# Kernel optimization log

Measured on AMD Instinct MI355X. Metric: run time of the kernel, lower is better.

The kernel has to match this reference:

```python
import jax, jax.numpy as jnp
import numpy as np

N = 50000      # nodes
E = 800000     # edges
G = 50         # graphs in batch
F_IN = 64      # num_node_features
HID = 128      # hidden_dim
EMB = 64       # embed_dim
H1 = 8         # heads layer 1
C1 = HID // H1 # per-head channels layer 1
NCLS = 6
EPS = 1e-5
NEG_SLOPE = 0.2


def setup_inputs() -> dict:
    key = jax.random.key(0)
    ks = jax.random.split(key, 26)
    rn = lambda k, s, sc=0.1: jax.random.normal(k, s, jnp.float32) * sc
    return {
        "x": jax.random.normal(ks[0], (N, F_IN), jnp.float32),
        "edge_index": jax.random.randint(ks[1], (2, E), 0, N),
        "edge_attr": jax.random.uniform(ks[2], (E, 1), dtype=jnp.float32),
        "batch": jnp.sort(jax.random.randint(ks[3], (N,), 0, G)),
        # conv1 (GATv2, heads=8, concat)
        "Wl1": rn(ks[4], (F_IN, HID)), "bl1": jnp.zeros((HID,), jnp.float32),
        "Wr1": rn(ks[5], (F_IN, HID)), "br1": jnp.zeros((HID,), jnp.float32),
        "We1": rn(ks[6], (1, HID)),
        "att1": rn(ks[7], (H1, C1)), "bias1": jnp.zeros((HID,), jnp.float32),
        # conv2 (GATv2, heads=1, mean)
        "Wl2": rn(ks[8], (HID, EMB)), "bl2": jnp.zeros((EMB,), jnp.float32),
        "Wr2": rn(ks[9], (HID, EMB)), "br2": jnp.zeros((EMB,), jnp.float32),
        "We2": rn(ks[10], (1, EMB)),
        "att2": rn(ks[11], (1, EMB)), "bias2": jnp.zeros((EMB,), jnp.float32),
        # batchnorms
        "gamma1": jnp.ones((HID,), jnp.float32), "beta1": jnp.zeros((HID,), jnp.float32),
        "gamma2": jnp.ones((EMB,), jnp.float32), "beta2": jnp.zeros((EMB,), jnp.float32),
        # classifier
        "Wc": rn(ks[12], (EMB, NCLS)), "bc": jnp.zeros((NCLS,), jnp.float32),
    }


def _segment_softmax(logits, seg, n):
    # logits: [E, H], softmax over edges sharing the same destination node
    m = jax.ops.segment_max(logits, seg, num_segments=n)
    e = jnp.exp(logits - m[seg])
    s = jax.ops.segment_sum(e, seg, num_segments=n)
    return e / s[seg]


def _gatv2(x, src, dst, eattr, Wl, bl, Wr, br, We, att, bias, H, C, concat):
    n = x.shape[0]
    xl = (x @ Wl + bl).reshape(n, H, C)   # source transform (messages)
    xr = (x @ Wr + br).reshape(n, H, C)   # target transform
    ee = (eattr @ We).reshape(-1, H, C)   # edge feature embedding
    g = jax.nn.leaky_relu(xl[src] + xr[dst] + ee, NEG_SLOPE)  # [E,H,C]
    alpha = jnp.einsum('ehc,hc->eh', g, att)                  # [E,H]
    alpha = _segment_softmax(alpha, dst, n)
    out = jax.ops.segment_sum(xl[src] * alpha[:, :, None], dst, num_segments=n)
    out = out.reshape(n, H * C) if concat else out.mean(axis=1)
    return out + bias


def _add_self_loops(edge_index, eattr, n):
    # PyG add_self_loops with fill_value='mean': self-loop edge_attr = mean of
    # incoming edge_attr per node (0 if isolated)
    src, dst = edge_index[0], edge_index[1]
    deg = jax.ops.segment_sum(jnp.ones((src.shape[0],), jnp.float32), dst, num_segments=n)
    s = jax.ops.segment_sum(eattr, dst, num_segments=n)
    loop_attr = jnp.where(deg[:, None] > 0, s / jnp.maximum(deg, 1.0)[:, None], 0.0)
    ar = jnp.arange(n)
    return (jnp.concatenate([src, ar]), jnp.concatenate([dst, ar]),
            jnp.concatenate([eattr, loop_attr], axis=0))


def _bn_train(x, gamma, beta):
    mu = x.mean(axis=0)
    var = x.var(axis=0)  # biased, as BatchNorm uses for normalization
    return (x - mu) * jax.lax.rsqrt(var + EPS) * gamma + beta


def reference(x, edge_index, edge_attr, batch,
              Wl1, bl1, Wr1, br1, We1, att1, bias1,
              Wl2, bl2, Wr2, br2, We2, att2, bias2,
              gamma1, beta1, gamma2, beta2, Wc, bc):
    src, dst, ea = _add_self_loops(edge_index, edge_attr, N)
    h = _gatv2(x, src, dst, ea, Wl1, bl1, Wr1, br1, We1, att1, bias1, H1, C1, True)
    h = jax.nn.relu(_bn_train(h, gamma1, beta1))
    h = _gatv2(h, src, dst, ea, Wl2, bl2, Wr2, br2, We2, att2, bias2, 1, EMB, False)
    node_emb = jax.nn.relu(_bn_train(h, gamma2, beta2))
    cnt = jax.ops.segment_sum(jnp.ones((N,), jnp.float32), batch, num_segments=G)
    domain_emb = jax.ops.segment_sum(node_emb, batch, num_segments=G) / jnp.maximum(cnt, 1.0)[:, None]
    logits = domain_emb @ Wc + bc
    return (logits, domain_emb, node_emb)
```

## Files before the change

kernel.cpp:

```cpp
#include <hip/hip_runtime.h>
#include <hip/hip_bf16.h>
#include <math.h>

#define NN 50000
#define EE 800000
#define GG 50
#define FIN 64
#define HID 128
#define EMB 64
#define NCLS 6
#define EPSBN 1e-5f
#define NEG 0.2f
#define MAXD 64

__device__ __forceinline__ float lrelu(float x){ return x > 0.f ? x : NEG * x; }
__device__ __forceinline__ float bf16lo(unsigned u){ return __uint_as_float(u << 16); }
__device__ __forceinline__ float bf16hi(unsigned u){ return __uint_as_float(u & 0xffff0000u); }
__device__ __forceinline__ unsigned f2bf_bits(float f){
    unsigned u = __float_as_uint(f);
    return (u + 0x7fffu + ((u >> 16) & 1u)) >> 16;
}

__global__ void k_scatter(const int* __restrict__ ei, const float* __restrict__ ea,
                          unsigned long long* __restrict__ combo,
                          unsigned* __restrict__ epack) {
    int e = blockIdx.x * 256 + threadIdx.x;
    if (e < EE) {
        int d = ei[EE + e];
        int s = ei[e];
        float eaf = ea[e];
        unsigned long long add = (1ULL << 40) | (unsigned long long)(eaf * 1048576.0f);
        unsigned long long old = atomicAdd(&combo[d], add);
        int pos = (int)(old >> 40);
        epack[d * MAXD + pos] = ((unsigned)s << 16) | f2bf_bits(eaf);
    }
}

__global__ void k_decode(const unsigned long long* __restrict__ combo,
                         int* __restrict__ deg, float* __restrict__ loopattr) {
    int n = blockIdx.x * 256 + threadIdx.x;
    if (n < NN) {
        unsigned long long c = combo[n];
        int cnt = (int)(c >> 40);
        float easum = (float)(c & ((1ULL << 40) - 1)) * (1.0f / 1048576.0f);
        deg[n] = cnt;
        loopattr[n] = cnt > 0 ? easum / (float)cnt : 0.f;
    }
}

__global__ void k_bounds(const int* __restrict__ batch, int* __restrict__ gstart) {
    int n = blockIdx.x * 256 + threadIdx.x;
    if (n < NN) {
        int b = batch[n];
        int prev = (n == 0) ? -1 : batch[n - 1];
        for (int g = prev + 1; g <= b; g++) gstart[g] = n;
        if (n == NN - 1) {
            for (int g = b + 1; g <= GG; g++) gstart[g] = NN;
        }
    }
}

#define G1R 8
__global__ void k_gemm1(const float* __restrict__ x,
                        const float* __restrict__ Wl, const float* __restrict__ bl,
                        const float* __restrict__ Wr, const float* __restrict__ br,
                        __hip_bfloat16* __restrict__ xlh, float* __restrict__ xr) {
    __shared__ float xs[G1R][FIN];
    int rb = blockIdx.x * G1R;
    int t = threadIdx.x;
    for (int i = t; i < G1R * FIN; i += 256) {
        int r = i >> 6, k = i & 63;
        xs[r][k] = x[(rb + r) * FIN + k];
    }
    __syncthreads();
    bool isL = t < HID;
    int c = isL ? t : t - HID;
    const float* W = isL ? Wl : Wr;
    float bias = isL ? bl[c] : br[c];
    float acc[G1R];
#pragma unroll
    for (int r = 0; r < G1R; r++) acc[r] = bias;
    for (int k = 0; k < FIN; k++) {
        float w = W[k * HID + c];
#pragma unroll
        for (int r = 0; r < G1R; r++) acc[r] += xs[r][k] * w;
    }
    if (isL) {
#pragma unroll
        for (int r = 0; r < G1R; r++) xlh[(rb + r) * HID + c] = __float2bfloat16(acc[r]);
    } else {
#pragma unroll
        for (int r = 0; r < G1R; r++) xr[(rb + r) * HID + c] = acc[r];
    }
}

__global__ void k_gat1(const float* __restrict__ loopattr, const int* __restrict__ deg,
                       const unsigned* __restrict__ epack,
                       const __hip_bfloat16* __restrict__ xlh, const float* __restrict__ xr1,
                       const float* __restrict__ We1, const float* __restrict__ att1,
                       const float* __restrict__ bias1, float* __restrict__ out1) {
    int wid = (blockIdx.x * blockDim.x + threadIdx.x) >> 6;
    int lane = threadIdx.x & 63;
    if (wid >= NN) return;
    int n = wid;
    int half = lane >> 5;
    int cl   = lane & 31;
    int c0   = 4 * cl;
    float4 xrv = *reinterpret_cast<const float4*>(&xr1[n * HID + c0]);
    float4 we  = *reinterpret_cast<const float4*>(&We1[c0]);
    float4 at  = *reinterpret_cast<const float4*>(&att1[c0]);
    float la = loopattr[n];
    int beg = n * MAXD, end = beg + deg[n];

    float m0 = -INFINITY, s0 = 0.f, a00 = 0.f, a01 = 0.f, a02 = 0.f, a03 = 0.f;
    float m1 = -INFINITY, s1 = 0.f, a10 = 0.f, a11 = 0.f, a12 = 0.f, a13 = 0.f;

#define UPD1(U, EA, MM, SS, A0, A1, A2, A3)                                   \
    {                                                                          \
        float x0 = bf16lo((U).x), x1 = bf16hi((U).x);                          \
        float x2 = bf16lo((U).y), x3 = bf16hi((U).y);                          \
        float g0 = lrelu(x0 + xrv.x + (EA) * we.x);                            \
        float g1 = lrelu(x1 + xrv.y + (EA) * we.y);                            \
        float g2 = lrelu(x2 + xrv.z + (EA) * we.z);                            \
        float g3 = lrelu(x3 + xrv.w + (EA) * we.w);                            \
        float part = g0 * at.x + g1 * at.y + g2 * at.z + g3 * at.w;            \
        part += __shfl_xor(part, 1);                                           \
        part += __shfl_xor(part, 2);                                           \
        float mnew = fmaxf(MM, part);                                          \
        float sc = __expf(MM - mnew);                                          \
        float p  = __expf(part - mnew);                                        \
        SS = SS * sc + p;                                                      \
        A0 = A0 * sc + x0 * p;                                                 \
        A1 = A1 * sc + x1 * p;                                                 \
        A2 = A2 * sc + x2 * p;                                                 \
        A3 = A3 * sc + x3 * p;                                                 \
        MM = mnew;                                                             \
    }

    for (int base = beg; base < end; base += 4) {
        int i0 = base + half;
        int i1 = i0 + 2;
        bool act0 = i0 < end;
        bool act1 = i1 < end;
        unsigned q0 = act0 ? epack[i0] : 0u;
        unsigned q1 = act1 ? epack[i1] : 0u;
        uint2 u0 = act0 ? *reinterpret_cast<const uint2*>(&xlh[(q0 >> 16) * HID + c0]) : make_uint2(0, 0);
        uint2 u1 = act1 ? *reinterpret_cast<const uint2*>(&xlh[(q1 >> 16) * HID + c0]) : make_uint2(0, 0);
        if (act0) UPD1(u0, bf16lo(q0), m0, s0, a00, a01, a02, a03);
        if (act1) UPD1(u1, bf16lo(q1), m1, s1, a10, a11, a12, a13);
    }
    if (half == 1) {
        uint2 u = *reinterpret_cast<const uint2*>(&xlh[n * HID + c0]);
        UPD1(u, la, m0, s0, a00, a01, a02, a03);
    }
#undef UPD1

    {
        float mm = fmaxf(m0, m1);
        float e0 = (m0 > -INFINITY) ? __expf(m0 - mm) : 0.f;
        float e1 = (m1 > -INFINITY) ? __expf(m1 - mm) : 0.f;
        s0 = s0 * e0 + s1 * e1;
        a00 = a00 * e0 + a10 * e1;
        a01 = a01 * e0 + a11 * e1;
        a02 = a02 * e0 + a12 * e1;
        a03 = a03 * e0 + a13 * e1;
        m0 = mm;
    }
    {
        float mo = __shfl_xor(m0, 32);
        float so = __shfl_xor(s0, 32);
        float b0 = __shfl_xor(a00, 32);
        float b1 = __shfl_xor(a01, 32);
        float b2 = __shfl_xor(a02, 32);
        float b3 = __shfl_xor(a03, 32);
        float mm = fmaxf(m0, mo);
        float e0 = (m0 > -INFINITY) ? __expf(m0 - mm) : 0.f;
        float e1 = (mo > -INFINITY) ? __expf(mo - mm) : 0.f;
        s0 = s0 * e0 + so * e1;
        a00 = a00 * e0 + b0 * e1;
        a01 = a01 * e0 + b1 * e1;
        a02 = a02 * e0 + b2 * e1;
        a03 = a03 * e0 + b3 * e1;
    }
    if (half == 0) {
        float4 bi = *reinterpret_cast<const float4*>(&bias1[c0]);
        float inv = 1.f / s0;
        float4 o = make_float4(a00 * inv + bi.x, a01 * inv + bi.y,
                               a02 * inv + bi.z, a03 * inv + bi.w);
        *reinterpret_cast<float4*>(&out1[n * HID + c0]) = o;
    }
}

template <int CH>
__global__ void k_bnstat(const float* __restrict__ xin, float* __restrict__ sums,
                         float* __restrict__ sumsq) {
    constexpr int RPI = 256 / CH;
    int t = threadIdx.x;
    int c = t % CH;
    int rl = t / CH;
    float s = 0.f, q = 0.f;
    for (int r = blockIdx.x * RPI + rl; r < NN; r += gridDim.x * RPI) {
        float v = xin[r * CH + c];
        s += v; q += v * v;
    }
    __shared__ float sh[256], shq[256];
    sh[t] = s; shq[t] = q;
    __syncthreads();
    if (t < CH) {
        float ts = 0.f, tq = 0.f;
        for (int i = t; i < 256; i += CH) { ts += sh[i]; tq += shq[i]; }
        atomicAdd(&sums[c], ts);
        atomicAdd(&sumsq[c], tq);
    }
}

template <int CH>
__global__ void k_bnfin(const float* __restrict__ sums, const float* __restrict__ sumsq,
                        const float* __restrict__ gamma, const float* __restrict__ beta,
                        float* __restrict__ a, float* __restrict__ b) {
    int c = threadIdx.x;
    if (c < CH) {
        float mean = sums[c] / (float)NN;
        float var  = sumsq[c] / (float)NN - mean * mean;
        float rs = rsqrtf(var + EPSBN);
        float aa = gamma[c] * rs;
        a[c] = aa;
        b[c] = beta[c] - mean * aa;
    }
}

#define G2R 8
__global__ void k_gemm2(const float* __restrict__ out1, const float* __restrict__ a1,
                        const float* __restrict__ b1,
                        const float* __restrict__ Wl, const float* __restrict__ bl,
                        const float* __restrict__ Wr, const float* __restrict__ br,
                        __hip_bfloat16* __restrict__ xlh, float* __restrict__ xr2) {
    __shared__ float hs[G2R][HID];
    int rb = blockIdx.x * G2R;
    int t = threadIdx.x;
    for (int i = t; i < G2R * HID; i += 256) {
        int r = i >> 7, k = i & 127;
        float v = out1[(rb + r) * HID + k] * a1[k] + b1[k];
        hs[r][k] = v > 0.f ? v : 0.f;
    }
    __syncthreads();
    int c = t & 127;
    int rg = (t >> 7) * 4;
    bool isL = c < EMB;
    int cc = isL ? c : c - EMB;
    const float* W = isL ? Wl : Wr;
    float bias = isL ? bl[cc] : br[cc];
    float acc[4] = {bias, bias, bias, bias};
    for (int k = 0; k < HID; k++) {
        float w = W[k * EMB + cc];
#pragma unroll
        for (int r = 0; r < 4; r++) acc[r] += hs[rg + r][k] * w;
    }
    if (isL) {
#pragma unroll
        for (int r = 0; r < 4; r++) xlh[(rb + rg + r) * EMB + cc] = __float2bfloat16(acc[r]);
    } else {
#pragma unroll
        for (int r = 0; r < 4; r++) xr2[(rb + rg + r) * EMB + cc] = acc[r];
    }
}

__global__ void k_gat2(const float* __restrict__ loopattr, const int* __restrict__ deg,
                       const unsigned* __restrict__ epack,
                       const __hip_bfloat16* __restrict__ xlh, const float* __restrict__ xr2,
                       const float* __restrict__ We2, const float* __restrict__ att2,
                       const float* __restrict__ bias2, float* __restrict__ out2) {
    int wid = (blockIdx.x * blockDim.x + threadIdx.x) >> 6;
    int lane = threadIdx.x & 63;
    if (wid >= NN) return;
    int n = wid;
    int half = lane >> 5;
    int cl   = lane & 31;
    int c0   = 2 * cl;
    float2 xrv = *reinterpret_cast<const float2*>(&xr2[n * EMB + c0]);
    float2 we  = *reinterpret_cast<const float2*>(&We2[c0]);
    float2 at  = *reinterpret_cast<const float2*>(&att2[c0]);
    float la = loopattr[n];
    int beg = n * MAXD, end = beg + deg[n];

    float m0 = -INFINITY, s0 = 0.f, a00 = 0.f, a01 = 0.f;
    float m1 = -INFINITY, s1 = 0.f, a10 = 0.f, a11 = 0.f;

#define UPD2(U, EA, MM, SS, A0, A1)                                           \
    {                                                                          \
        float x0 = bf16lo(U), x1 = bf16hi(U);                                  \
        float g0 = lrelu(x0 + xrv.x + (EA) * we.x);                            \
        float g1 = lrelu(x1 + xrv.y + (EA) * we.y);                            \
        float part = g0 * at.x + g1 * at.y;                                    \
        part += __shfl_xor(part, 1);                                           \
        part += __shfl_xor(part, 2);                                           \
        part += __shfl_xor(part, 4);                                           \
        part += __shfl_xor(part, 8);                                           \
        part += __shfl_xor(part, 16);                                          \
        float mnew = fmaxf(MM, part);                                          \
        float sc = __expf(MM - mnew);                                          \
        float p  = __expf(part - mnew);                                        \
        SS = SS * sc + p;                                                      \
        A0 = A0 * sc + x0 * p;                                                 \
        A1 = A1 * sc + x1 * p;                                                 \
        MM = mnew;                                                             \
    }

    for (int base = beg; base < end; base += 4) {
        int i0 = base + half;
        int i1 = i0 + 2;
        bool act0 = i0 < end;
        bool act1 = i1 < end;
        unsigned q0 = act0 ? epack[i0] : 0u;
        unsigned q1 = act1 ? epack[i1] : 0u;
        unsigned u0 = act0 ? *reinterpret_cast<const unsigned*>(&xlh[(q0 >> 16) * EMB + c0]) : 0u;
        unsigned u1 = act1 ? *reinterpret_cast<const unsigned*>(&xlh[(q1 >> 16) * EMB + c0]) : 0u;
        if (act0) UPD2(u0, bf16lo(q0), m0, s0, a00, a01);
        if (act1) UPD2(u1, bf16lo(q1), m1, s1, a10, a11);
    }
    if (half == 1) {
        unsigned u = *reinterpret_cast<const unsigned*>(&xlh[n * EMB + c0]);
        UPD2(u, la, m0, s0, a00, a01);
    }
#undef UPD2

    {
        float mm = fmaxf(m0, m1);
        float e0 = (m0 > -INFINITY) ? __expf(m0 - mm) : 0.f;
        float e1 = (m1 > -INFINITY) ? __expf(m1 - mm) : 0.f;
        s0 = s0 * e0 + s1 * e1;
        a00 = a00 * e0 + a10 * e1;
        a01 = a01 * e0 + a11 * e1;
        m0 = mm;
    }
    {
        float mo = __shfl_xor(m0, 32);
        float so = __shfl_xor(s0, 32);
        float b0 = __shfl_xor(a00, 32);
        float b1 = __shfl_xor(a01, 32);
        float mm = fmaxf(m0, mo);
        float e0 = (m0 > -INFINITY) ? __expf(m0 - mm) : 0.f;
        float e1 = (mo > -INFINITY) ? __expf(mo - mm) : 0.f;
        s0 = s0 * e0 + so * e1;
        a00 = a00 * e0 + b0 * e1;
        a01 = a01 * e0 + b1 * e1;
    }
    if (half == 0) {
        float inv = 1.f / s0;
        float2 o = make_float2(a00 * inv + bias2[c0], a01 * inv + bias2[c0 + 1]);
        *reinterpret_cast<float2*>(&out2[n * EMB + c0]) = o;
    }
}

__global__ void k_emb(const float* __restrict__ out2, const float* __restrict__ a2,
                      const float* __restrict__ b2, float* __restrict__ nodeemb) {
    int i = blockIdx.x * 256 + threadIdx.x;
    if (i < NN * EMB) {
        int c = i & 63;
        float v = out2[i] * a2[c] + b2[c];
        nodeemb[i] = v > 0.f ? v : 0.f;
    }
}

__global__ void k_pool(const float* __restrict__ nodeemb, const int* __restrict__ gstart,
                       const float* __restrict__ Wc, const float* __restrict__ bc,
                       float* __restrict__ dom, float* __restrict__ logits) {
    int g = blockIdx.x;
    int t = threadIdx.x;
    int c = t & 63, rl = t >> 6;
    int beg = gstart[g], end = gstart[g + 1];
    float s = 0.f;
    for (int r = beg + rl; r < end; r += 4) s += nodeemb[r * EMB + c];
    __shared__ float sh[256];
    __shared__ float dsh[EMB];
    sh[t] = s;
    __syncthreads();
    if (t < EMB) {
        float tot = sh[t] + sh[t + 64] + sh[t + 128] + sh[t + 192];
        float cf = (float)(end - beg);
        if (cf < 1.f) cf = 1.f;
        float d = tot / cf;
        dsh[t] = d;
        dom[g * EMB + t] = d;
    }
    __syncthreads();
    if (t < NCLS) {
        float acc = bc[t];
        for (int k = 0; k < EMB; k++) acc += dsh[k] * Wc[k * NCLS + t];
        logits[g * NCLS + t] = acc;
    }
}

extern "C" void kernel_launch(void* const* d_in, const int* in_sizes, int n_in,
                              void* d_out, int out_size, void* d_ws, size_t ws_size,
                              hipStream_t stream) {
    const float* x     = (const float*)d_in[0];
    const int*   ei    = (const int*)d_in[1];
    const float* ea    = (const float*)d_in[2];
    const int*   batch = (const int*)d_in[3];
    const float* Wl1 = (const float*)d_in[4];
    const float* bl1 = (const float*)d_in[5];
    const float* Wr1 = (const float*)d_in[6];
    const float* br1 = (const float*)d_in[7];
    const float* We1 = (const float*)d_in[8];
    const float* att1 = (const float*)d_in[9];
    const float* bias1 = (const float*)d_in[10];
    const float* Wl2 = (const float*)d_in[11];
    const float* bl2 = (const float*)d_in[12];
    const float* Wr2 = (const float*)d_in[13];
    const float* br2 = (const float*)d_in[14];
    const float* We2 = (const float*)d_in[15];
    const float* att2 = (const float*)d_in[16];
    const float* bias2 = (const float*)d_in[17];
    const float* gamma1 = (const float*)d_in[18];
    const float* beta1  = (const float*)d_in[19];
    const float* gamma2 = (const float*)d_in[20];
    const float* beta2  = (const float*)d_in[21];
    const float* Wc = (const float*)d_in[22];
    const float* bc = (const float*)d_in[23];

    float* out_logits = (float*)d_out;
    float* out_dom    = out_logits + GG * NCLS;
    float* out_emb    = out_dom + GG * EMB;

    char* ws = (char*)d_ws;
    const size_t SZF = (size_t)NN * HID * sizeof(float);
    const size_t SZH = (size_t)NN * HID * sizeof(__hip_bfloat16);
    const size_t SZE = (size_t)NN * MAXD * sizeof(unsigned);
    __hip_bfloat16* xl1h = (__hip_bfloat16*)(ws);
    float* xr1  = (float*)(ws + SZH);
    float* out1 = (float*)(ws + SZH + SZF);
    __hip_bfloat16* xl2h = xl1h;
    float* xr2  = xr1;
    float* out2 = out1;
    unsigned* epack = (unsigned*)(ws + SZH + 2 * SZF);
    int*   deg      = (int*)(ws + SZH + 2 * SZF + SZE);
    float* loopattr = (float*)(deg + NN);
    unsigned long long* combo = (unsigned long long*)(loopattr + NN);
    float* sums1  = (float*)(combo + NN);
    float* sumsq1 = sums1 + HID;
    float* sums2  = sumsq1 + HID;
    float* sumsq2 = sums2 + EMB;
    size_t zero_bytes = (char*)(sumsq2 + EMB) - (char*)combo;
    float* a1 = (float*)(sumsq2 + EMB);
    float* b1 = a1 + HID;
    float* a2 = b1 + HID;
    float* b2 = a2 + EMB;
    int* gstart = (int*)(b2 + EMB);

    hipMemsetAsync(combo, 0, zero_bytes, stream);

    k_scatter<<<(EE + 255) / 256, 256, 0, stream>>>(ei, ea, combo, epack);
    k_decode<<<(NN + 255) / 256, 256, 0, stream>>>(combo, deg, loopattr);
    k_bounds<<<(NN + 255) / 256, 256, 0, stream>>>(batch, gstart);

    k_gemm1<<<NN / G1R, 256, 0, stream>>>(x, Wl1, bl1, Wr1, br1, xl1h, xr1);
    k_gat1<<<(NN * 64) / 256, 256, 0, stream>>>(loopattr, deg, epack,
                                                xl1h, xr1, We1, att1, bias1, out1);
    k_bnstat<HID><<<1024, 256, 0, stream>>>(out1, sums1, sumsq1);
    k_bnfin<HID><<<1, HID, 0, stream>>>(sums1, sumsq1, gamma1, beta1, a1, b1);
    k_gemm2<<<NN / G2R, 256, 0, stream>>>(out1, a1, b1, Wl2, bl2, Wr2, br2, xl2h, xr2);
    k_gat2<<<(NN * 64) / 256, 256, 0, stream>>>(loopattr, deg, epack,
                                                xl2h, xr2, We2, att2, bias2, out2);
    k_bnstat<EMB><<<1024, 256, 0, stream>>>(out2, sums2, sumsq2);
    k_bnfin<EMB><<<1, EMB, 0, stream>>>(sums2, sumsq2, gamma2, beta2, a2, b2);
    k_emb<<<(NN * EMB + 255) / 256, 256, 0, stream>>>(out2, a2, b2, out_emb);
    k_pool<<<GG, 256, 0, stream>>>(out_emb, gstart, Wc, bc, out_dom, out_logits);
}
```

Before: 499.3 us.

## Drop online-softmax max tracking, fuse decode/bounds, and fuse emb with pooling

Removes the running-max rescaling in both GAT aggregation kernels and accumulates exp(logit) directly, which makes the half-wave and cross-half merges plain sums. Merges the degree decode and graph-bounds kernels into one launch. Folds the BN2 apply and ReLU into a parallel pooling kernel (several blocks per graph, atomics into a zeroed buffer) followed by a small logits kernel, so the node-embedding pass is no longer split across two launches. Skipping the max subtraction risks exp overflow for large attention logits, and the float atomics make the pooled sums order-dependent.

New measurement: 443.0 us. 11.3% less time.

```diff
diff --git a/kernel.cpp b/kernel.cpp
--- a/kernel.cpp
+++ b/kernel.cpp
@@ -12,6 +12,7 @@
 #define EPSBN 1e-5f
 #define NEG 0.2f
 #define MAXD 64
+#define PB 8
 
 __device__ __forceinline__ float lrelu(float x){ return x > 0.f ? x : NEG * x; }
 __device__ __forceinline__ float bf16lo(unsigned u){ return __uint_as_float(u << 16); }
@@ -36,8 +37,9 @@
     }
 }
 
-__global__ void k_decode(const unsigned long long* __restrict__ combo,
-                         int* __restrict__ deg, float* __restrict__ loopattr) {
+__global__ void k_prep(const unsigned long long* __restrict__ combo,
+                       int* __restrict__ deg, float* __restrict__ loopattr,
+                       const int* __restrict__ batch, int* __restrict__ gstart) {
     int n = blockIdx.x * 256 + threadIdx.x;
     if (n < NN) {
         unsigned long long c = combo[n];
@@ -45,12 +47,6 @@
         float easum = (float)(c & ((1ULL << 40) - 1)) * (1.0f / 1048576.0f);
         deg[n] = cnt;
         loopattr[n] = cnt > 0 ? easum / (float)cnt : 0.f;
-    }
-}
-
-__global__ void k_bounds(const int* __restrict__ batch, int* __restrict__ gstart) {
-    int n = blockIdx.x * 256 + threadIdx.x;
-    if (n < NN) {
         int b = batch[n];
         int prev = (n == 0) ? -1 : batch[n - 1];
         for (int g = prev + 1; g <= b; g++) gstart[g] = n;
@@ -112,10 +108,10 @@
     float la = loopattr[n];
     int beg = n * MAXD, end = beg + deg[n];
 
-    float m0 = -INFINITY, s0 = 0.f, a00 = 0.f, a01 = 0.f, a02 = 0.f, a03 = 0.f;
-    float m1 = -INFINITY, s1 = 0.f, a10 = 0.f, a11 = 0.f, a12 = 0.f, a13 = 0.f;
-
-#define UPD1(U, EA, MM, SS, A0, A1, A2, A3)                                   \
+    float s0 = 0.f, a00 = 0.f, a01 = 0.f, a02 = 0.f, a03 = 0.f;
+    float s1 = 0.f, a10 = 0.f, a11 = 0.f, a12 = 0.f, a13 = 0.f;
+
+#define UPD1(U, EA, SS, A0, A1, A2, A3)                                       \
     {                                                                          \
         float x0 = bf16lo((U).x), x1 = bf16hi((U).x);                          \
         float x2 = bf16lo((U).y), x3 = bf16hi((U).y);                          \
@@ -126,15 +122,12 @@
         float part = g0 * at.x + g1 * at.y + g2 * at.z + g3 * at.w;            \
         part += __shfl_xor(part, 1);                                           \
         part += __shfl_xor(part, 2);                                           \
-        float mnew = fmaxf(MM, part);                                          \
-        float sc = __expf(MM - mnew);                                          \
-        float p  = __expf(part - mnew);                                        \
-        SS = SS * sc + p;                                                      \
-        A0 = A0 * sc + x0 * p;                                                 \
-        A1 = A1 * sc + x1 * p;                                                 \
-        A2 = A2 * sc + x2 * p;                                                 \
-        A3 = A3 * sc + x3 * p;                                                 \
-        MM = mnew;                                                             \
+        float p = __expf(part);                                                \
+        SS += p;                                                               \
+        A0 = fmaf(x0, p, A0);                                                  \
+        A1 = fmaf(x1, p, A1);                                                  \
+        A2 = fmaf(x2, p, A2);                                                  \
+        A3 = fmaf(x3, p, A3);                                                  \
     }
 
     for (int base = beg; base < end; base += 4) {
@@ -146,42 +139,21 @@
         unsigned q1 = act1 ? epack[i1] : 0u;
         uint2 u0 = act0 ? *reinterpret_cast<const uint2*>(&xlh[(q0 >> 16) * HID + c0]) : make_uint2(0, 0);
         uint2 u1 = act1 ? *reinterpret_cast<const uint2*>(&xlh[(q1 >> 16) * HID + c0]) : make_uint2(0, 0);
-        if (act0) UPD1(u0, bf16lo(q0), m0, s0, a00, a01, a02, a03);
-        if (act1) UPD1(u1, bf16lo(q1), m1, s1, a10, a11, a12, a13);
+        if (act0) UPD1(u0, bf16lo(q0), s0, a00, a01, a02, a03);
+        if (act1) UPD1(u1, bf16lo(q1), s1, a10, a11, a12, a13);
     }
     if (half == 1) {
         uint2 u = *reinterpret_cast<const uint2*>(&xlh[n * HID + c0]);
-        UPD1(u, la, m0, s0, a00, a01, a02, a03);
+        UPD1(u, la, s0, a00, a01, a02, a03);
     }
 #undef UPD1
 
-    {
-        float mm = fmaxf(m0, m1);
-        float e0 = (m0 > -INFINITY) ? __expf(m0 - mm) : 0.f;
-        float e1 = (m1 > -INFINITY) ? __expf(m1 - mm) : 0.f;
-        s0 = s0 * e0 + s1 * e1;
-        a00 = a00 * e0 + a10 * e1;
-        a01 = a01 * e0 + a11 * e1;
-        a02 = a02 * e0 + a12 * e1;
-        a03 = a03 * e0 + a13 * e1;
-        m0 = mm;
-    }
-    {
-        float mo = __shfl_xor(m0, 32);
-        float so = __shfl_xor(s0, 32);
-        float b0 = __shfl_xor(a00, 32);
-        float b1 = __shfl_xor(a01, 32);
-        float b2 = __shfl_xor(a02, 32);
-        float b3 = __shfl_xor(a03, 32);
-        float mm = fmaxf(m0, mo);
-        float e0 = (m0 > -INFINITY) ? __expf(m0 - mm) : 0.f;
-        float e1 = (mo > -INFINITY) ? __expf(mo - mm) : 0.f;
-        s0 = s0 * e0 + so * e1;
-        a00 = a00 * e0 + b0 * e1;
-        a01 = a01 * e0 + b1 * e1;
-        a02 = a02 * e0 + b2 * e1;
-        a03 = a03 * e0 + b3 * e1;
-    }
+    s0 += s1; a00 += a10; a01 += a11; a02 += a12; a03 += a13;
+    s0  += __shfl_xor(s0, 32);
+    a00 += __shfl_xor(a00, 32);
+    a01 += __shfl_xor(a01, 32);
+    a02 += __shfl_xor(a02, 32);
+    a03 += __shfl_xor(a03, 32);
     if (half == 0) {
         float4 bi = *reinterpret_cast<const float4*>(&bias1[c0]);
         float inv = 1.f / s0;
@@ -283,10 +255,10 @@
     float la = loopattr[n];
     int beg = n * MAXD, end = beg + deg[n];
 
-    float m0 = -INFINITY, s0 = 0.f, a00 = 0.f, a01 = 0.f;
-    float m1 = -INFINITY, s1 = 0.f, a10 = 0.f, a11 = 0.f;
-
-#define UPD2(U, EA, MM, SS, A0, A1)                                           \
+    float s0 = 0.f, a00 = 0.f, a01 = 0.f;
+    float s1 = 0.f, a10 = 0.f, a11 = 0.f;
+
+#define UPD2(U, EA, SS, A0, A1)                                               \
     {                                                                          \
         float x0 = bf16lo(U), x1 = bf16hi(U);                                  \
         float g0 = lrelu(x0 + xrv.x + (EA) * we.x);                            \
@@ -297,13 +269,10 @@
         part += __shfl_xor(part, 4);                                           \
         part += __shfl_xor(part, 8);                                           \
         part += __shfl_xor(part, 16);                                          \
-        float mnew = fmaxf(MM, part);                                          \
-        float sc = __expf(MM - mnew);                                          \
-        float p  = __expf(part - mnew);                                        \
-        SS = SS * sc + p;                                                      \
-        A0 = A0 * sc + x0 * p;                                                 \
-        A1 = A1 * sc + x1 * p;                                                 \
-        MM = mnew;                                                             \
+        float p = __expf(part);                                                \
+        SS += p;                                                               \
+        A0 = fmaf(x0, p, A0);                                                  \
+        A1 = fmaf(x1, p, A1);                                                  \
     }
 
     for (int base = beg; base < end; base += 4) {
@@ -315,36 +284,19 @@
         unsigned q1 = act1 ? epack[i1] : 0u;
         unsigned u0 = act0 ? *reinterpret_cast<const unsigned*>(&xlh[(q0 >> 16) * EMB + c0]) : 0u;
         unsigned u1 = act1 ? *reinterpret_cast<const unsigned*>(&xlh[(q1 >> 16) * EMB + c0]) : 0u;
-        if (act0) UPD2(u0, bf16lo(q0), m0, s0, a00, a01);
-        if (act1) UPD2(u1, bf16lo(q1), m1, s1, a10, a11);
+        if (act0) UPD2(u0, bf16lo(q0), s0, a00, a01);
+        if (act1) UPD2(u1, bf16lo(q1), s1, a10, a11);
     }
     if (half == 1) {
         unsigned u = *reinterpret_cast<const unsigned*>(&xlh[n * EMB + c0]);
-        UPD2(u, la, m0, s0, a00, a01);
+        UPD2(u, la, s0, a00, a01);
     }
 #undef UPD2
 
-    {
-        float mm = fmaxf(m0, m1);
-        float e0 = (m0 > -INFINITY) ? __expf(m0 - mm) : 0.f;
-        float e1 = (m1 > -INFINITY) ? __expf(m1 - mm) : 0.f;
-        s0 = s0 * e0 + s1 * e1;
-        a00 = a00 * e0 + a10 * e1;
-        a01 = a01 * e0 + a11 * e1;
-        m0 = mm;
-    }
-    {
-        float mo = __shfl_xor(m0, 32);
-        float so = __shfl_xor(s0, 32);
-        float b0 = __shfl_xor(a00, 32);
-        float b1 = __shfl_xor(a01, 32);
-        float mm = fmaxf(m0, mo);
-        float e0 = (m0 > -INFINITY) ? __expf(m0 - mm) : 0.f;
-        float e1 = (mo > -INFINITY) ? __expf(mo - mm) : 0.f;
-        s0 = s0 * e0 + so * e1;
-        a00 = a00 * e0 + b0 * e1;
-        a01 = a01 * e0 + b1 * e1;
-    }
+    s0 += s1; a00 += a10; a01 += a11;
+    s0  += __shfl_xor(s0, 32);
+    a00 += __shfl_xor(a00, 32);
+    a01 += __shfl_xor(a01, 32);
     if (half == 0) {
         float inv = 1.f / s0;
         float2 o = make_float2(a00 * inv + bias2[c0], a01 * inv + bias2[c0 + 1]);
@@ -352,37 +304,41 @@
     }
 }
 
-__global__ void k_emb(const float* __restrict__ out2, const float* __restrict__ a2,
-                      const float* __restrict__ b2, float* __restrict__ nodeemb) {
-    int i = blockIdx.x * 256 + threadIdx.x;
-    if (i < NN * EMB) {
-        int c = i & 63;
-        float v = out2[i] * a2[c] + b2[c];
-        nodeemb[i] = v > 0.f ? v : 0.f;
-    }
-}
-
-__global__ void k_pool(const float* __restrict__ nodeemb, const int* __restrict__ gstart,
-                       const float* __restrict__ Wc, const float* __restrict__ bc,
-                       float* __restrict__ dom, float* __restrict__ logits) {
-    int g = blockIdx.x;
+__global__ void k_poolA(const float* __restrict__ out2, const float* __restrict__ a2,
+                        const float* __restrict__ b2, const int* __restrict__ gstart,
+                        float* __restrict__ nodeemb, float* __restrict__ domsum) {
+    int g = blockIdx.x / PB;
+    int sb = blockIdx.x % PB;
     int t = threadIdx.x;
     int c = t & 63, rl = t >> 6;
     int beg = gstart[g], end = gstart[g + 1];
     float s = 0.f;
-    for (int r = beg + rl; r < end; r += 4) s += nodeemb[r * EMB + c];
+    for (int r = beg + sb * 4 + rl; r < end; r += PB * 4) {
+        float v = out2[r * EMB + c] * a2[c] + b2[c];
+        v = v > 0.f ? v : 0.f;
+        nodeemb[r * EMB + c] = v;
+        s += v;
+    }
     __shared__ float sh[256];
-    __shared__ float dsh[EMB];
     sh[t] = s;
     __syncthreads();
     if (t < EMB) {
         float tot = sh[t] + sh[t + 64] + sh[t + 128] + sh[t + 192];
-        float cf = (float)(end - beg);
-        if (cf < 1.f) cf = 1.f;
-        float d = tot / cf;
-        dsh[t] = d;
-        dom[g * EMB + t] = d;
-    }
+        atomicAdd(&domsum[g * EMB + t], tot);
+    }
+}
+
+__global__ void k_logits(const float* __restrict__ domsum, const int* __restrict__ gstart,
+                         const float* __restrict__ Wc, const float* __restrict__ bc,
+                         float* __restrict__ dom, float* __restrict__ logits) {
+    int g = blockIdx.x;
+    int t = threadIdx.x;
+    __shared__ float dsh[EMB];
+    float cf = (float)(gstart[g + 1] - gstart[g]);
+    if (cf < 1.f) cf = 1.f;
+    float d = domsum[g * EMB + t] / cf;
+    dsh[t] = d;
+    dom[g * EMB + t] = d;
     __syncthreads();
     if (t < NCLS) {
         float acc = bc[t];
@@ -441,8 +397,9 @@
     float* sumsq1 = sums1 + HID;
     float* sums2  = sumsq1 + HID;
     float* sumsq2 = sums2 + EMB;
-    size_t zero_bytes = (char*)(sumsq2 + EMB) - (char*)combo;
-    float* a1 = (float*)(sumsq2 + EMB);
+    float* domsum = sumsq2 + EMB;
+    size_t zero_bytes = (char*)(domsum + GG * EMB) - (char*)combo;
+    float* a1 = domsum + GG * EMB;
     float* b1 = a1 + HID;
     float* a2 = b1 + HID;
     float* b2 = a2 + EMB;
@@ -451,8 +408,7 @@
     hipMemsetAsync(combo, 0, zero_bytes, stream);
 
     k_scatter<<<(EE + 255) / 256, 256, 0, stream>>>(ei, ea, combo, epack);
-    k_decode<<<(NN + 255) / 256, 256, 0, stream>>>(combo, deg, loopattr);
-    k_bounds<<<(NN + 255) / 256, 256, 0, stream>>>(batch, gstart);
+    k_prep<<<(NN + 255) / 256, 256, 0, stream>>>(combo, deg, loopattr, batch, gstart);
 
     k_gemm1<<<NN / G1R, 256, 0, stream>>>(x, Wl1, bl1, Wr1, br1, xl1h, xr1);
     k_gat1<<<(NN * 64) / 256, 256, 0, stream>>>(loopattr, deg, epack,
@@ -464,6 +420,6 @@
                                                 xl2h, xr2, We2, att2, bias2, out2);
     k_bnstat<EMB><<<1024, 256, 0, stream>>>(out2, sums2, sumsq2);
     k_bnfin<EMB><<<1, EMB, 0, stream>>>(sums2, sumsq2, gamma2, beta2, a2, b2);
-    k_emb<<<(NN * EMB + 255) / 256, 256, 0, stream>>>(out2, a2, b2, out_emb);
-    k_pool<<<GG, 256, 0, stream>>>(out_emb, gstart, Wc, bc, out_dom, out_logits);
-}
+    k_poolA<<<GG * PB, 256, 0, stream>>>(out2, a2, b2, gstart, out_emb, domsum);
+    k_logits<<<GG, EMB, 0, stream>>>(domsum, gstart, Wc, bc, out_dom, out_logits);
+}
```
